# Kernel tuning notes

Hardware: AMD Instinct MI355X
Metric: run time of the kernel (lower is better)

The kernel has to match this reference:

```python
import jax, jax.numpy as jnp
import numpy as np

EMBED_DIM = 1024
NUM_HEADS = 16
HEAD_DIM = EMBED_DIM // NUM_HEADS


def setup_inputs() -> dict:
    key = jax.random.key(0)
    kx, kq, kk, kv, kbq, kbk, kbv = jax.random.split(key, 7)
    s = 1.0 / np.sqrt(EMBED_DIM)
    return {
        "x": jax.random.normal(kx, (4, 2048, EMBED_DIM), dtype=jnp.float32),
        "Wq": jax.random.uniform(kq, (EMBED_DIM, EMBED_DIM), jnp.float32, -s, s),
        "bq": jax.random.uniform(kbq, (EMBED_DIM,), jnp.float32, -s, s),
        "Wk": jax.random.uniform(kk, (EMBED_DIM, EMBED_DIM), jnp.float32, -s, s),
        "bk": jax.random.uniform(kbk, (EMBED_DIM,), jnp.float32, -s, s),
        "Wv": jax.random.uniform(kv, (EMBED_DIM, EMBED_DIM), jnp.float32, -s, s),
        "bv": jax.random.uniform(kbv, (EMBED_DIM,), jnp.float32, -s, s),
    }


def reference(x, Wq, bq, Wk, bk, Wv, bv):
    B, S, E = x.shape
    H, D = NUM_HEADS, HEAD_DIM
    # QKV projections; reshape to (B, H, S, D)
    def proj(W, b):
        return (x @ W + b).reshape(B, S, H, D).transpose(0, 2, 1, 3)
    Q = proj(Wq, bq)
    K = proj(Wk, bk)
    V = proj(Wv, bv)
    scale = jnp.asarray(np.sqrt(D), x.dtype)
    scores = jnp.einsum("bhqd,bhkd->bhqk", Q, K) / scale
    attn = jax.nn.softmax(scores, axis=-1)
    out = jnp.einsum("bhqk,bhkd->bhqd", attn, V)
    return out.transpose(0, 2, 1, 3).reshape(B, S, E)
```

## Files before the change

### kernel.cpp

```cpp
#include <hip/hip_runtime.h>
#include <math.h>

typedef unsigned short u16;
typedef __bf16 bf16x8 __attribute__((ext_vector_type(8)));
typedef float f32x4 __attribute__((ext_vector_type(4)));
typedef u16 u16x8 __attribute__((ext_vector_type(8)));
typedef u16 u16x4 __attribute__((ext_vector_type(4)));
typedef short s16x4 __attribute__((ext_vector_type(4)));
typedef unsigned u32x2 __attribute__((ext_vector_type(2)));
typedef unsigned u32x4 __attribute__((ext_vector_type(4)));

#define BB 4
#define SS 2048
#define EE 1024
#define HH 16
#define DH 64
#define PLANE (SS * DH)

__device__ __forceinline__ u16 f32_to_bf16(float f) {
  unsigned u = __builtin_bit_cast(unsigned, f);
  u += 0x7fffu + ((u >> 16) & 1u);
  return (u16)(u >> 16);
}

__device__ __forceinline__ unsigned pack_bf16_trunc(float lo, float hi) {
  return __builtin_amdgcn_perm(__builtin_bit_cast(unsigned, hi),
                               __builtin_bit_cast(unsigned, lo), 0x07060302u);
}

__device__ __forceinline__ void async_copy16(const void* g, void* lds) {
  __builtin_amdgcn_global_load_lds(
      (const __attribute__((address_space(1))) void*)g,
      (__attribute__((address_space(3))) void*)lds, 16, 0, 0);
}

__device__ __forceinline__ float ex2(float x) {
#if __has_builtin(__builtin_amdgcn_exp2f)
  return __builtin_amdgcn_exp2f(x);
#else
  return exp2f(x);
#endif
}

__global__ void cvt_x_kernel(const float* __restrict__ x, u16* __restrict__ xb) {
  int i = (blockIdx.x * 256 + threadIdx.x) * 8;
  float4 a = *(const float4*)(x + i);
  float4 c = *(const float4*)(x + i + 4);
  u16x8 o;
  o[0] = f32_to_bf16(a.x); o[1] = f32_to_bf16(a.y);
  o[2] = f32_to_bf16(a.z); o[3] = f32_to_bf16(a.w);
  o[4] = f32_to_bf16(c.x); o[5] = f32_to_bf16(c.y);
  o[6] = f32_to_bf16(c.z); o[7] = f32_to_bf16(c.w);
  *(u16x8*)(xb + i) = o;
}

__global__ void cvt_w_kernel(const float* __restrict__ Wq, const float* __restrict__ Wk,
                             const float* __restrict__ Wv, u16* __restrict__ wb) {
  __shared__ u16 T[64 * 72];
  int mat = blockIdx.z;
  const float* W = (mat == 0) ? Wq : ((mat == 1) ? Wk : Wv);
  int e0 = blockIdx.x * 64, k0 = blockIdx.y * 64;
  int t = threadIdx.x;
  int tr = t >> 4, tc = t & 15;
  for (int i = 0; i < 4; ++i) {
    int k = i * 16 + tr;
    float4 v = *(const float4*)(W + (k0 + k) * EE + e0 + tc * 4);
    T[(tc * 4 + 0) * 72 + k] = f32_to_bf16(v.x);
    T[(tc * 4 + 1) * 72 + k] = f32_to_bf16(v.y);
    T[(tc * 4 + 2) * 72 + k] = f32_to_bf16(v.z);
    T[(tc * 4 + 3) * 72 + k] = f32_to_bf16(v.w);
  }
  __syncthreads();
  u16* out = wb + (size_t)(mat * EE + e0) * EE + k0;
  for (int i = 0; i < 4; ++i) {
    int e = i * 16 + tr;
    u16x4 v = *(u16x4*)&T[e * 72 + tc * 4];
    *(u16x4*)(out + e * EE + tc * 4) = v;
  }
}

__global__ __launch_bounds__(256) void qkv_gemm_kernel(
    const u16* __restrict__ A, const u16* __restrict__ Bt,
    const float* __restrict__ bq, const float* __restrict__ bk,
    const float* __restrict__ bv, u16* __restrict__ qkv) {
  __shared__ u16 As[128 * 32];
  __shared__ u16 Bs[128 * 32];
  int tid = threadIdx.x;
  int lane = tid & 63, w = tid >> 6;
  int ln = lane & 15, quad = lane >> 4;
  int wm = w & 1, wn = w >> 1;
  int bn = blockIdx.x, bm = blockIdx.y;
  const u16* Ag = A + (size_t)bm * 128 * EE;
  const u16* Bg = Bt + (size_t)bn * 128 * EE;

  f32x4 acc[4][4] = {};

  for (int kt = 0; kt < 32; ++kt) {
    int k0 = kt * 32;
    __syncthreads();
    for (int i = 0; i < 2; ++i) {
      int c = w * 128 + i * 64 + lane;
      int row = c >> 2, kc = (c & 3) * 8;
      async_copy16(Ag + row * EE + k0 + kc, &As[(w * 128 + i * 64) * 8]);
      async_copy16(Bg + row * EE + k0 + kc, &Bs[(w * 128 + i * 64) * 8]);
    }
    __syncthreads();
    bf16x8 af[4], bfr[4];
    for (int mi = 0; mi < 4; ++mi)
      af[mi] = *(const bf16x8*)&As[(wm * 64 + mi * 16 + ln) * 32 + quad * 8];
    for (int ni = 0; ni < 4; ++ni)
      bfr[ni] = *(const bf16x8*)&Bs[(wn * 64 + ni * 16 + ln) * 32 + quad * 8];
    for (int mi = 0; mi < 4; ++mi)
      for (int ni = 0; ni < 4; ++ni)
        acc[mi][ni] = __builtin_amdgcn_mfma_f32_16x16x32_bf16(af[mi], bfr[ni],
                                                              acc[mi][ni], 0, 0, 0);
  }

  int mat = bn >> 3;
  const float* bias = (mat == 0) ? bq : ((mat == 1) ? bk : bv);
  int b = bm >> 4;
  if (mat < 2) {
    float scl = (mat == 0) ? 0.18033688011112042f : 1.0f;
    int base0 = (mat * BB + b) * HH * PLANE;
    for (int ni = 0; ni < 4; ++ni) {
      int e = (bn & 7) * 128 + wn * 64 + ni * 16 + ln;
      float bve = bias[e];
      int hh = e >> 6, d = e & 63;
      int cb = base0 + hh * PLANE + d;
      for (int mi = 0; mi < 4; ++mi) {
        int s0 = (bm & 15) * 128 + wm * 64 + mi * 16 + quad * 4;
        for (int r = 0; r < 4; ++r)
          qkv[cb + (s0 + r) * DH] = f32_to_bf16((acc[mi][ni][r] + bve) * scl);
      }
    }
  } else {
    size_t base0 = (size_t)(2 * BB + b) * HH * PLANE;
    for (int ni = 0; ni < 4; ++ni) {
      int e = (bn & 7) * 128 + wn * 64 + ni * 16 + ln;
      float bve = bias[e];
      int hh = e >> 6, d = e & 63;
      size_t cb = base0 + (size_t)hh * PLANE + (size_t)d * SS;
      for (int mi = 0; mi < 4; ++mi) {
        int s0 = (bm & 15) * 128 + wm * 64 + mi * 16 + quad * 4;
        u16x4 vv;
        for (int r = 0; r < 4; ++r) vv[r] = f32_to_bf16(acc[mi][ni][r] + bve);
        *(u16x4*)(qkv + cb + s0) = vv;
      }
    }
  }
}

__global__ __launch_bounds__(256, 4) void attn_kernel(const u16* __restrict__ qkv,
                                                      float* __restrict__ out) {
  __shared__ u16 Ks0[64 * 64], Ks1[64 * 64];
  __shared__ u16 Vs0[64 * 64], Vs1[64 * 64];
  int qb = blockIdx.x, h = blockIdx.y, b = blockIdx.z;
  int t = threadIdx.x;
  int lane = t & 63, w = t >> 6;
  int ln = lane & 15, quad = lane >> 4;
  int k7 = ln & 7;
  int q0 = quad & 1, q1 = quad >> 1;
  int bh = b * HH + h;
  const u16* Qg = qkv + (size_t)bh * PLANE + qb * 128 * DH;
  const u16* Kg = qkv + (size_t)(BB * HH + bh) * PLANE;
  const u16* Vg = qkv + (size_t)(2 * BB * HH + bh) * PLANE;

  int r8 = lane >> 3, c8 = lane & 7;
  int sc8 = (c8 ^ r8) * 8;

  auto STAGE = [&](u16* KsD, u16* VsD, int kt) {
    const u16* Kt = Kg + kt * 64 * DH;
    const u16* Vt = Vg + kt * 64;
#pragma unroll
    for (int i = 0; i < 2; ++i) {
      int row = w * 16 + i * 8 + r8;
      async_copy16(Kt + row * DH + sc8, KsD + (w * 16 + i * 8) * DH);
      async_copy16(Vt + row * SS + sc8, VsD + (w * 16 + i * 8) * DH);
    }
  };

  bf16x8 bq[2][2];
#pragma unroll
  for (int rb = 0; rb < 2; ++rb)
#pragma unroll
    for (int s = 0; s < 2; ++s)
      bq[rb][s] = *(const bf16x8*)(Qg + (w * 32 + rb * 16 + ln) * DH + s * 32 + quad * 8);

  u32x4 ow;
  ow[0] = ow[1] = ow[2] = ow[3] = 0x3F803F80u;
  bf16x8 ones8 = __builtin_bit_cast(bf16x8, ow);

  const f32x4 kz = {};
  f32x4 o[4][2] = {};
  f32x4 lacc[2] = {};

  int ks0 = (quad ^ k7) * 8;
  int ks1 = ks0 ^ 32;

  auto TILE = [&](const u16* Ksb, const u16* Vsb) {
    __builtin_amdgcn_s_setprio(1);
    f32x4 s[2][4];
#pragma unroll
    for (int g = 0; g < 4; ++g) {
      const u16* krow = Ksb + (g * 16 + ln) * DH;
      bf16x8 kf0 = *(const bf16x8*)(krow + ks0);
      bf16x8 kf1 = *(const bf16x8*)(krow + ks1);
      s[0][g] = __builtin_amdgcn_mfma_f32_16x16x32_bf16(kf0, bq[0][0], kz, 0, 0, 0);
      s[0][g] = __builtin_amdgcn_mfma_f32_16x16x32_bf16(kf1, bq[0][1], s[0][g], 0, 0, 0);
      s[1][g] = __builtin_amdgcn_mfma_f32_16x16x32_bf16(kf0, bq[1][0], kz, 0, 0, 0);
      s[1][g] = __builtin_amdgcn_mfma_f32_16x16x32_bf16(kf1, bq[1][1], s[1][g], 0, 0, 0);
    }
    bf16x8 af[2][2];
#pragma unroll
    for (int rb = 0; rb < 2; ++rb) {
      unsigned Wd[4][2];
#pragma unroll
      for (int g = 0; g < 4; ++g) {
        Wd[g][0] = pack_bf16_trunc(ex2(s[rb][g][0]), ex2(s[rb][g][1]));
        Wd[g][1] = pack_bf16_trunc(ex2(s[rb][g][2]), ex2(s[rb][g][3]));
      }
#pragma unroll
      for (int G = 0; G < 2; ++G) {
        u32x4 aw;
        aw[0] = Wd[2 * G][0];     aw[1] = Wd[2 * G][1];
        aw[2] = Wd[2 * G + 1][0]; aw[3] = Wd[2 * G + 1][1];
        af[rb][G] = __builtin_bit_cast(bf16x8, aw);
      }
      lacc[rb] = __builtin_amdgcn_mfma_f32_16x16x32_bf16(af[rb][0], ones8, lacc[rb], 0, 0, 0);
      lacc[rb] = __builtin_amdgcn_mfma_f32_16x16x32_bf16(af[rb][1], ones8, lacc[rb], 0, 0, 0);
    }
#pragma unroll
    for (int G = 0; G < 2; ++G) {
      int uLo = ((4 * G + q1) ^ k7) * 8 + 4 * q0;
      int uHi = ((4 * G + q1 + 2) ^ k7) * 8 + 4 * q0;
#pragma unroll
      for (int dg = 0; dg < 4; ++dg) {
        const u16* vrow = Vsb + (dg * 16 + ln) * DH;
        u32x2 lo = *(const u32x2*)(vrow + uLo);
        u32x2 hi = *(const u32x2*)(vrow + uHi);
        u32x4 vv;
        vv[0] = lo[0]; vv[1] = lo[1]; vv[2] = hi[0]; vv[3] = hi[1];
        bf16x8 vf = __builtin_bit_cast(bf16x8, vv);
        o[dg][0] = __builtin_amdgcn_mfma_f32_16x16x32_bf16(af[0][G], vf, o[dg][0], 0, 0, 0);
        o[dg][1] = __builtin_amdgcn_mfma_f32_16x16x32_bf16(af[1][G], vf, o[dg][1], 0, 0, 0);
      }
    }
    __builtin_amdgcn_s_setprio(0);
  };

  STAGE(Ks0, Vs0, 0);
#pragma unroll 1
  for (int kt = 0; kt < 32; kt += 2) {
    STAGE(Ks1, Vs1, kt + 1);
    asm volatile("s_waitcnt vmcnt(4)" ::: "memory");
    __builtin_amdgcn_sched_barrier(0);
    __builtin_amdgcn_s_barrier();
    __builtin_amdgcn_sched_barrier(0);
    TILE(Ks0, Vs0);
    __builtin_amdgcn_s_barrier();
    if (kt + 2 < 32) {
      STAGE(Ks0, Vs0, kt + 2);
      asm volatile("s_waitcnt vmcnt(4)" ::: "memory");
    } else {
      asm volatile("s_waitcnt vmcnt(0)" ::: "memory");
    }
    __builtin_amdgcn_sched_barrier(0);
    __builtin_amdgcn_s_barrier();
    __builtin_amdgcn_sched_barrier(0);
    TILE(Ks1, Vs1);
    __builtin_amdgcn_s_barrier();
  }

  int sb = qb * 128 + w * 32;
  float* og = out + (size_t)b * SS * EE + (size_t)h * DH;
#pragma unroll
  for (int rb = 0; rb < 2; ++rb)
#pragma unroll
    for (int r = 0; r < 4; ++r) {
      float ir = 1.0f / lacc[rb][r];
      size_t qrow = (size_t)(sb + rb * 16 + quad * 4 + r);
#pragma unroll
      for (int dg = 0; dg < 4; ++dg)
        og[qrow * EE + dg * 16 + ln] = o[dg][rb][r] * ir;
    }
}

extern "C" void kernel_launch(void* const* d_in, const int* in_sizes, int n_in,
                              void* d_out, int out_size, void* d_ws, size_t ws_size,
                              hipStream_t stream) {
  (void)in_sizes; (void)n_in; (void)out_size; (void)ws_size;
  const float* x  = (const float*)d_in[0];
  const float* Wq = (const float*)d_in[1];
  const float* bq = (const float*)d_in[2];
  const float* Wk = (const float*)d_in[3];
  const float* bk = (const float*)d_in[4];
  const float* Wv = (const float*)d_in[5];
  const float* bv = (const float*)d_in[6];
  float* out = (float*)d_out;

  u16* xb  = (u16*)d_out;
  u16* wb  = xb + (size_t)BB * SS * EE;
  u16* qkv = (u16*)d_ws;

  cvt_x_kernel<<<dim3((BB * SS * EE) / (256 * 8)), 256, 0, stream>>>(x, xb);
  cvt_w_kernel<<<dim3(16, 16, 3), 256, 0, stream>>>(Wq, Wk, Wv, wb);
  qkv_gemm_kernel<<<dim3(24, 64), 256, 0, stream>>>(xb, wb, bq, bk, bv, qkv);
  attn_kernel<<<dim3(SS / 128, HH, BB), 256, 0, stream>>>(qkv, out);
}
```

Before: 248.7 us.

## Double-buffer QKV GEMM LDS tiles with async prefetch and swizzle block order

Restructures the QKV projection GEMM main loop to use two LDS buffers, issuing the async global-to-LDS copy for the next K-tile before computing the current one and waiting with explicit vmcnt counts. This is meant to hide global load latency behind MFMA work. It also remaps workgroup IDs so consecutive blocks share B tiles for better L2 reuse, and raises wave priority during the MFMA section. The cost is doubled LDS use, which may lower occupancy, and a dependence on correct hand-written waitcnt counts.

```diff
diff --git a/kernel.cpp b/kernel.cpp
--- a/kernel.cpp
+++ b/kernel.cpp
@@ -83,37 +83,70 @@
     const u16* __restrict__ A, const u16* __restrict__ Bt,
     const float* __restrict__ bq, const float* __restrict__ bk,
     const float* __restrict__ bv, u16* __restrict__ qkv) {
-  __shared__ u16 As[128 * 32];
-  __shared__ u16 Bs[128 * 32];
+  __shared__ u16 As0[128 * 32], Bs0[128 * 32];
+  __shared__ u16 As1[128 * 32], Bs1[128 * 32];
   int tid = threadIdx.x;
   int lane = tid & 63, w = tid >> 6;
   int ln = lane & 15, quad = lane >> 4;
   int wm = w & 1, wn = w >> 1;
-  int bn = blockIdx.x, bm = blockIdx.y;
+  int wg = blockIdx.y * 24 + blockIdx.x;
+  int swz = (wg & 7) * 192 + (wg >> 3);
+  int bn = swz % 24, bm = swz / 24;
   const u16* Ag = A + (size_t)bm * 128 * EE;
   const u16* Bg = Bt + (size_t)bn * 128 * EE;
 
   f32x4 acc[4][4] = {};
 
-  for (int kt = 0; kt < 32; ++kt) {
+  auto STAGE = [&](u16* AsD, u16* BsD, int kt) {
     int k0 = kt * 32;
-    __syncthreads();
+#pragma unroll
     for (int i = 0; i < 2; ++i) {
       int c = w * 128 + i * 64 + lane;
       int row = c >> 2, kc = (c & 3) * 8;
-      async_copy16(Ag + row * EE + k0 + kc, &As[(w * 128 + i * 64) * 8]);
-      async_copy16(Bg + row * EE + k0 + kc, &Bs[(w * 128 + i * 64) * 8]);
-    }
-    __syncthreads();
+      async_copy16(Ag + row * EE + k0 + kc, AsD + (w * 128 + i * 64) * 8);
+      async_copy16(Bg + row * EE + k0 + kc, BsD + (w * 128 + i * 64) * 8);
+    }
+  };
+
+  auto TILE = [&](const u16* AsB, const u16* BsB) {
+    __builtin_amdgcn_s_setprio(1);
     bf16x8 af[4], bfr[4];
+#pragma unroll
     for (int mi = 0; mi < 4; ++mi)
-      af[mi] = *(const bf16x8*)&As[(wm * 64 + mi * 16 + ln) * 32 + quad * 8];
+      af[mi] = *(const bf16x8*)&AsB[(wm * 64 + mi * 16 + ln) * 32 + quad * 8];
+#pragma unroll
     for (int ni = 0; ni < 4; ++ni)
-      bfr[ni] = *(const bf16x8*)&Bs[(wn * 64 + ni * 16 + ln) * 32 + quad * 8];
+      bfr[ni] = *(const bf16x8*)&BsB[(wn * 64 + ni * 16 + ln) * 32 + quad * 8];
+#pragma unroll
     for (int mi = 0; mi < 4; ++mi)
+#pragma unroll
       for (int ni = 0; ni < 4; ++ni)
         acc[mi][ni] = __builtin_amdgcn_mfma_f32_16x16x32_bf16(af[mi], bfr[ni],
                                                               acc[mi][ni], 0, 0, 0);
+    __builtin_amdgcn_s_setprio(0);
+  };
+
+  STAGE(As0, Bs0, 0);
+#pragma unroll 1
+  for (int kt = 0; kt < 32; kt += 2) {
+    STAGE(As1, Bs1, kt + 1);
+    asm volatile("s_waitcnt vmcnt(4)" ::: "memory");
+    __builtin_amdgcn_sched_barrier(0);
+    __builtin_amdgcn_s_barrier();
+    __builtin_amdgcn_sched_barrier(0);
+    TILE(As0, Bs0);
+    __builtin_amdgcn_s_barrier();
+    if (kt + 2 < 32) {
+      STAGE(As0, Bs0, kt + 2);
+      asm volatile("s_waitcnt vmcnt(4)" ::: "memory");
+    } else {
+      asm volatile("s_waitcnt vmcnt(0)" ::: "memory");
+    }
+    __builtin_amdgcn_sched_barrier(0);
+    __builtin_amdgcn_s_barrier();
+    __builtin_amdgcn_sched_barrier(0);
+    TILE(As1, Bs1);
+    __builtin_amdgcn_s_barrier();
   }
 
   int mat = bn >> 3;
```

Result: no change. 247.2 us (-0.6%).
